# Performance work log

Measured on AMD Instinct MI355X. Metric: run time of the kernel, lower is better.

## Reference

```python
import jax, jax.numpy as jnp
import numpy as np

D_MODEL = 2048
NUM_HEADS = 16
MAX_SEQ_LEN = 2048
ROPE_BASE = 10000.0


def _rope(x, start_pos):
    # x: [B, S, D]; rotates interleaved pairs then concatenates halves,
    # exactly matching the torch module (NOT the usual interleaved output).
    B, S, D = x.shape
    theta = 1.0 / (ROPE_BASE ** (jnp.arange(0, D, 2, dtype=jnp.float32) / D))  # [D/2]
    pos = jnp.arange(start_pos, start_pos + S, dtype=jnp.float32)[:, None]      # [S,1]
    ang = pos * theta[None, :]                                                  # [S, D/2]
    cos, sin = jnp.cos(ang), jnp.sin(ang)
    x1 = x[..., 0::2]
    x2 = x[..., 1::2]
    return jnp.concatenate([x1 * cos - x2 * sin, x1 * sin + x2 * cos], axis=-1)


def setup_inputs() -> dict:
    key = jax.random.key(0)
    kx, kq, kk, kv, ko = jax.random.split(key, 5)
    B, S, D = 4, 2048, D_MODEL
    scale = 1.0 / np.sqrt(D)
    return {
        "x": jax.random.normal(kx, (B, S, D), dtype=jnp.float32),
        "w_q": jax.random.normal(kq, (D, D), dtype=jnp.float32) * scale,
        "w_k": jax.random.normal(kk, (D, D), dtype=jnp.float32) * scale,
        "w_v": jax.random.normal(kv, (D, D), dtype=jnp.float32) * scale,
        "w_o": jax.random.normal(ko, (D, D), dtype=jnp.float32) * scale,
        "start_pos": 0,
    }


def reference(x, w_q, w_k, w_v, w_o, start_pos):
    B, S, D = x.shape
    H = NUM_HEADS
    hd = D // H
    # Linear(d, d, bias=False): y = x @ W^T
    Q = _rope(x @ w_q.T, start_pos)
    K = _rope(x @ w_k.T, start_pos)
    V = x @ w_v.T
    q = Q.reshape(B, S, H, hd).transpose(0, 2, 1, 3)  # [B,H,S,hd]
    k = K.reshape(B, S, H, hd).transpose(0, 2, 1, 3)
    v = V.reshape(B, S, H, hd).transpose(0, 2, 1, 3)
    # cache=None path: kv_len == S
    attn = jnp.einsum("bhqd,bhkd->bhqk", q, k) / jnp.sqrt(jnp.float32(hd))
    # causal mask: key j attends only if j <= i + (kv_len - seq_len); here offset=0
    kv_len = k.shape[2]
    offset = kv_len - S
    i = jnp.arange(S)[:, None]
    j = jnp.arange(kv_len)[None, :]
    attn = jnp.where(j > i + offset, jnp.float32(-jnp.inf), attn)
    attn = jax.nn.softmax(attn, axis=-1)
    # dropout: inference mode (identity)
    out = jnp.einsum("bhqk,bhkd->bhqd", attn, v)
    out = out.transpose(0, 2, 1, 3).reshape(B, S, D)
    output = out @ w_o.T
    return (output, k, v)
```

## Files before the change

### kernel.cpp

```cpp
#include <hip/hip_runtime.h>
#include <hip/hip_bf16.h>

typedef __attribute__((ext_vector_type(4))) float f32x4;
typedef __attribute__((ext_vector_type(8))) short s16x8;

#define SEQ 2048
#define DM  2048
#define NH  16
#define HD  128

__device__ __forceinline__ unsigned short f2b(float f){
  unsigned int u = __builtin_bit_cast(unsigned int, f);
  u += 0x7fffu + ((u >> 16) & 1u);
  return (unsigned short)(u >> 16);
}
__device__ __forceinline__ float b2f(unsigned short h){
  unsigned int u = ((unsigned int)h) << 16;
  return __builtin_bit_cast(float, u);
}
__device__ __forceinline__ f32x4 mfma16(s16x8 a, s16x8 b, f32x4 c){
  return __builtin_amdgcn_mfma_f32_16x16x32_bf16(a, b, c, 0, 0, 0);
}

__global__ __launch_bounds__(256)
void convert_kernel(const float* __restrict__ x,  const float* __restrict__ wq,
                    const float* __restrict__ wk, const float* __restrict__ wv,
                    const float* __restrict__ wo,
                    unsigned short* __restrict__ xb,
                    unsigned short* __restrict__ wfused,
                    unsigned short* __restrict__ wob)
{
  size_t e = ((size_t)blockIdx.x * 256 + threadIdx.x) * 8;
  const float* src; unsigned short* dst;
  if (e < 16777216){ src = x + e; dst = xb + e; }
  else if (e < 29360128){
    size_t o = e - 16777216;
    int sel = (int)(o >> 22);
    const float* w = sel == 0 ? wq : (sel == 1 ? wk : wv);
    src = w + (o & 4194303); dst = wfused + o;
  } else {
    size_t o = e - 29360128;
    src = wo + o; dst = wob + o;
  }
  float4 a = ((const float4*)src)[0];
  float4 b = ((const float4*)src)[1];
  s16x8 v;
  v[0]=(short)f2b(a.x); v[1]=(short)f2b(a.y); v[2]=(short)f2b(a.z); v[3]=(short)f2b(a.w);
  v[4]=(short)f2b(b.x); v[5]=(short)f2b(b.y); v[6]=(short)f2b(b.z); v[7]=(short)f2b(b.w);
  *(s16x8*)dst = v;
}

template<int MODE>
__global__ __launch_bounds__(512, 1)
void gemm8(const unsigned short* __restrict__ A,
           const unsigned short* __restrict__ B,
           unsigned short* __restrict__ qr, unsigned short* __restrict__ kr,
           float* __restrict__ koutf,
           float* __restrict__ voutf, unsigned short* __restrict__ vt,
           float* __restrict__ outf, const int* __restrict__ sp)
{
  extern __shared__ char lds[];
  const int tid  = threadIdx.x;
  const int lane = tid & 63;
  const int w    = tid >> 6;
  const int wr   = w >> 2;
  const int wc   = w & 3;
  const int l15  = lane & 15;
  const int lhi  = lane >> 4;
  const int rq   = lhi << 2;

  int bid = blockIdx.x;
  int x8 = bid & 7, j = bid >> 3;
  int mb, nb;
  if (MODE == 0){ nb = 3*x8 + (j % 3); mb = j / 3; }
  else          { nb = x8;             mb = j; }
  const int m0 = mb * 256, n0 = nb * 256;

  const int sp0 = (MODE == 0) ? sp[0] : 0;

  const unsigned short* Abase = A + (size_t)m0 * 2048;
  const unsigned short* Bbase = B + (size_t)n0 * 2048;

  f32x4 accL[4][4] = {};
  f32x4 accH[4][4] = {};

  auto STAGE = [&](const unsigned short* gbase, int slotoff, int t){
    #pragma unroll
    for (int r2 = 0; r2 < 2; r2++){
      int p  = r2*8192 + w*1024 + (lane << 4);
      int lo = p ^ (((p >> 7) & 3) << 4);
      int row = lo >> 6, colB = lo & 63;
      __builtin_amdgcn_global_load_lds(
        (const __attribute__((address_space(1))) void*)
          (gbase + (size_t)row*2048 + t*32 + (colB >> 1)),
        (__attribute__((address_space(3))) void*)(lds + slotoff + r2*8192 + w*1024),
        16, 0, 0);
    }
  };
  auto LDA = [&](const char* base, int i0, s16x8* dst){
    #pragma unroll
    for (int i = 0; i < 4; i++){
      int row = wr*128 + (i0 + i)*16 + l15;
      int off = row*64 + lhi*16;
      dst[i] = *(const s16x8*)(base + (off ^ (((row >> 1) & 3) << 4)));
    }
  };
  auto LDB = [&](const char* base, s16x8* dst){
    #pragma unroll
    for (int j2 = 0; j2 < 4; j2++){
      int row = wc*64 + j2*16 + l15;
      int off = row*64 + lhi*16;
      dst[j2] = *(const s16x8*)(base + (off ^ (((row >> 1) & 3) << 4)));
    }
  };
  auto MM = [&](s16x8* a, s16x8* b, f32x4 (&ac)[4][4]){
    __builtin_amdgcn_s_setprio(1);
    #pragma unroll
    for (int i = 0; i < 4; i++)
      #pragma unroll
      for (int j2 = 0; j2 < 4; j2++)
        ac[i][j2] = mfma16(a[i], b[j2], ac[i][j2]);
    __builtin_amdgcn_s_setprio(0);
  };

#define TILE(T, ISSUE, VMW) { \
    const int s_ = (T) & 3; \
    const char* base_ = lds + s_*32768; \
    if (ISSUE){ \
      int so_ = (((T)+3) & 3)*32768; \
      STAGE(Abase, so_, (T)+3); \
      STAGE(Bbase, so_+16384, (T)+3); \
    } \
    s16x8 bfr[4], afL[4], afH[4]; \
    LDB(base_+16384, bfr); LDA(base_, 0, afL); LDA(base_, 4, afH); \
    MM(afL, bfr, accL); MM(afH, bfr, accH); \
    asm volatile("s_waitcnt vmcnt(" #VMW ")" ::: "memory"); \
    __builtin_amdgcn_s_barrier(); }

  STAGE(Abase, 0, 0);      STAGE(Bbase, 16384, 0);
  STAGE(Abase, 32768, 1);  STAGE(Bbase, 49152, 1);
  STAGE(Abase, 65536, 2);  STAGE(Bbase, 81920, 2);
  asm volatile("s_waitcnt vmcnt(8)" ::: "memory");
  __builtin_amdgcn_s_barrier();

  for (int t = 0; t < 61; t++) TILE(t, 1, 8);
  TILE(61, 0, 4);
  TILE(62, 0, 0);
  {
    const char* base_ = lds + 3*32768;
    s16x8 bfr[4], afL[4], afH[4];
    LDB(base_+16384, bfr); LDA(base_, 0, afL); LDA(base_, 4, afH);
    MM(afL, bfr, accL); MM(afH, bfr, accH);
  }
#undef TILE

  if (MODE == 1){
    #pragma unroll
    for (int h2 = 0; h2 < 2; h2++){
      f32x4 (&ac)[4][4] = h2 ? accH : accL;
      int ibase = h2 * 4;
      #pragma unroll
      for (int i = 0; i < 4; i++)
        #pragma unroll
        for (int r = 0; r < 4; r++){
          int m = m0 + wr*128 + (ibase+i)*16 + rq + r;
          #pragma unroll
          for (int j2 = 0; j2 < 4; j2++)
            outf[(size_t)m*DM + n0 + wc*64 + j2*16 + l15] = ac[i][j2][r];
        }
    }
    return;
  }

  const int b  = m0 >> 11;
  const int s0 = m0 & 2047;

  if (nb < 16){
    const bool isK = (nb >= 8);
    unsigned short* dqk = isK ? kr : qr;
    const int fbase = (nb & 7) * 128;
    const int odd = lane & 1;

    __syncthreads();
    float2* T2 = (float2*)lds;
    float2* T1 = (float2*)(lds + 32768);
    for (int idx = tid; idx < 5120; idx += 512){
      int fl = idx & 127;
      float th = exp2f(-(float)(fbase + fl) * (13.287712379549449f / 1024.0f));
      float sn, cn;
      if (idx < 4096){
        __sincosf((float)(idx >> 7) * th, &sn, &cn);
        T2[idx] = make_float2(cn, sn);
      } else {
        int sh = (idx - 4096) >> 7;
        __sincosf((float)(sp0 + s0 + sh*32) * th, &sn, &cn);
        T1[idx - 4096] = make_float2(cn, sn);
      }
    }
    __syncthreads();

    #pragma unroll
    for (int h2 = 0; h2 < 2; h2++){
      f32x4 (&ac)[4][4] = h2 ? accH : accL;
      int ibase = h2 * 4;
      #pragma unroll
      for (int i = 0; i < 4; i++){
        #pragma unroll
        for (int r = 0; r < 4; r++){
          int srow = wr*128 + (ibase+i)*16 + rq + r;
          int s  = s0 + srow;
          int sh = srow >> 5, sl = srow & 31;
          #pragma unroll
          for (int j2 = 0; j2 < 4; j2++){
            float v  = ac[i][j2][r];
            float vx = __shfl_xor(v, 1);
            int nn_loc = wc*64 + j2*16 + l15;
            int fl = nn_loc >> 1;
            float2 a1 = T1[sh*128 + fl];
            float2 a2 = T2[sl*128 + fl];
            float cn = a1.x*a2.x - a1.y*a2.y;
            float sn = a1.y*a2.x + a1.x*a2.y;
            float x1 = odd ? vx : v;
            float x2 = odd ? v  : vx;
            float ov = odd ? (x1*sn + x2*cn) : (x1*cn - x2*sn);
            int c = fbase + fl + (odd ? 1024 : 0);
            size_t adr = ((size_t)(b*NH + (c >> 7))*SEQ + s)*HD + (c & 127);
            dqk[adr] = f2b(ov);
            if (isK) koutf[adr] = ov;
          }
        }
      }
    }
  } else {
    #pragma unroll
    for (int h2 = 0; h2 < 2; h2++){
      f32x4 (&ac)[4][4] = h2 ? accH : accL;
      int ibase = h2 * 4;
      #pragma unroll
      for (int i = 0; i < 4; i++){
        int sb = s0 + wr*128 + (ibase+i)*16 + rq;
        #pragma unroll
        for (int j2 = 0; j2 < 4; j2++){
          int d = (nb - 16)*256 + wc*64 + j2*16 + l15;
          int h = d >> 7, dd = d & 127;
          size_t vb = ((size_t)(b*NH + h)*SEQ + sb)*HD + dd;
          #pragma unroll
          for (int r = 0; r < 4; r++)
            voutf[vb + (size_t)r*HD] = ac[i][j2][r];
          ushort4 pk;
          pk.x = f2b(ac[i][j2][0]); pk.y = f2b(ac[i][j2][1]);
          pk.z = f2b(ac[i][j2][2]); pk.w = f2b(ac[i][j2][3]);
          *(ushort4*)(vt + ((size_t)(b*NH + h)*HD + dd)*SEQ + sb) = pk;
        }
      }
    }
  }
}

__global__ __launch_bounds__(256)
void attn_kernel(const unsigned short* __restrict__ qr,
                 const unsigned short* __restrict__ kr,
                 const unsigned short* __restrict__ vt,
                 unsigned short* __restrict__ attnout)
{
  const int pair = blockIdx.x;
  const int bh   = blockIdx.y;
  const int tid  = threadIdx.x;
  const int lane = tid & 63;
  const int w    = tid >> 6;

  __shared__ __align__(16) char Klds[64 * 256];
  __shared__ __align__(16) char Vlds[128 * 144];
  __shared__ __align__(16) char Plds[4][16 * 144];

  const int l15 = lane & 15;
  const int lhi = lane >> 4;
  const int rq  = lhi << 2;
  char* pw = &Plds[w][0];

  s16x8 ones;
  #pragma unroll
  for (int i = 0; i < 8; i++) ones[i] = (short)0x3F80;

  const int b = bh >> 4, h = bh & 15;

  for (int ph = 0; ph < 2; ph++){
    const int qtile = ph ? (31 - pair) : pair;
    const int q0w = qtile*64 + w*16;

    s16x8 qf[4];
    const unsigned short* qbase = qr + ((size_t)bh*SEQ + q0w + l15) * HD + lhi*8;
    #pragma unroll
    for (int c = 0; c < 4; c++) qf[c] = *(const s16x8*)(qbase + c*32);

    f32x4 o[8] = {};
    f32x4 osum = {};
    float mrow[4] = {-1e30f,-1e30f,-1e30f,-1e30f};

    const int ntiles = qtile + 1;
    for (int t = 0; t < ntiles; t++){
      const int kv0 = t * 64;
      __syncthreads();
      {
        int r = tid >> 2, q4 = tid & 3;
        const unsigned short* src = kr + ((size_t)bh*SEQ + kv0 + r) * HD + q4*32;
        int sw = (r & 15) << 4;
        char* drow = Klds + r*256;
        #pragma unroll
        for (int k = 0; k < 4; k++)
          *(s16x8*)(drow + ((q4*64 + k*16) ^ sw)) = *(const s16x8*)(src + k*8);
      }
      {
        int r = tid >> 1, h2 = tid & 1;
        const unsigned short* src = vt + ((size_t)bh*HD + r) * SEQ + kv0 + h2*32;
        char* drow = Vlds + r*144 + h2*64;
        #pragma unroll
        for (int k = 0; k < 4; k++)
          *(s16x8*)(drow + k*16) = *(const s16x8*)(src + k*8);
      }
      __syncthreads();

      f32x4 st[4];
      #pragma unroll
      for (int j = 0; j < 4; j++) st[j] = (f32x4){0.f,0.f,0.f,0.f};
      #pragma unroll
      for (int j = 0; j < 4; j++){
        int krw = j*16 + l15;
        int sw  = (krw & 15) << 4;
        #pragma unroll
        for (int c = 0; c < 4; c++){
          s16x8 kf = *(const s16x8*)(Klds + krw*256 + ((c*64 + lhi*16) ^ sw));
          st[j] = mfma16(qf[c], kf, st[j]);
        }
      }

      const float sc = 0.08838834764831845f;
      #pragma unroll
      for (int j = 0; j < 4; j++)
        #pragma unroll
        for (int r = 0; r < 4; r++){
          int qrow = q0w + rq + r;
          int kvc  = kv0 + j*16 + l15;
          st[j][r] = (kvc > qrow) ? -1e30f : st[j][r] * sc;
        }

      float mt[4];
      #pragma unroll
      for (int r = 0; r < 4; r++)
        mt[r] = fmaxf(fmaxf(st[0][r], st[1][r]), fmaxf(st[2][r], st[3][r]));
      #pragma unroll
      for (int mk = 1; mk < 16; mk <<= 1)
        #pragma unroll
        for (int r = 0; r < 4; r++) mt[r] = fmaxf(mt[r], __shfl_xor(mt[r], mk));

      int ok = 1;
      #pragma unroll
      for (int r = 0; r < 4; r++) ok &= (mt[r] <= mrow[r] + 8.0f) ? 1 : 0;
      if (!__all(ok)){
        float al[4];
        #pragma unroll
        for (int r = 0; r < 4; r++){
          float mn = fmaxf(mrow[r], mt[r]);
          al[r] = __expf(mrow[r] - mn);
          mrow[r] = mn;
        }
        #pragma unroll
        for (int c = 0; c < 8; c++)
          #pragma unroll
          for (int r = 0; r < 4; r++) o[c][r] *= al[r];
        #pragma unroll
        for (int r = 0; r < 4; r++) osum[r] *= al[r];
      }

      #pragma unroll
      for (int r = 0; r < 4; r++){
        char* prb = pw + (rq + r)*144;
        #pragma unroll
        for (int j = 0; j < 4; j++){
          float p = __expf(st[j][r] - mrow[r]);
          *(unsigned short*)(prb + (j*16 + l15)*2) = f2b(p);
        }
      }

      asm volatile("s_waitcnt lgkmcnt(0)" ::: "memory");

      #pragma unroll
      for (int ks = 0; ks < 2; ks++){
        s16x8 pa = *(const s16x8*)(pw + l15*144 + ks*64 + lhi*16);
        #pragma unroll
        for (int c = 0; c < 8; c++){
          int d = c*16 + l15;
          s16x8 vf = *(const s16x8*)(Vlds + d*144 + ks*64 + lhi*16);
          o[c] = mfma16(pa, vf, o[c]);
        }
        osum = mfma16(pa, ones, osum);
      }
    }

    #pragma unroll
    for (int r = 0; r < 4; r++){
      float inv = 1.0f / osum[r];
      int s2 = q0w + rq + r;
      size_t base = ((size_t)(b*SEQ + s2)) * DM + h*HD;
      #pragma unroll
      for (int c = 0; c < 8; c++)
        attnout[base + c*16 + l15] = f2b(o[c][r] * inv);
    }
  }
}

extern "C" void kernel_launch(void* const* d_in, const int* in_sizes, int n_in,
                              void* d_out, int out_size, void* d_ws, size_t ws_size,
                              hipStream_t stream)
{
  const float* x  = (const float*)d_in[0];
  const float* wq = (const float*)d_in[1];
  const float* wk = (const float*)d_in[2];
  const float* wv = (const float*)d_in[3];
  const float* wo = (const float*)d_in[4];
  const int*   sp = (const int*)d_in[5];

  float* out  = (float*)d_out;
  float* kout = out + 16777216;
  float* vout = out + 33554432;

  char* ws = (char*)d_ws;
  unsigned short* xb      = (unsigned short*)ws;
  unsigned short* wfused  = (unsigned short*)(ws + 33554432);
  unsigned short* wob     = (unsigned short*)(ws + 58720256);
  unsigned short* qr      = (unsigned short*)(ws + 67108864);
  unsigned short* kr      = (unsigned short*)(ws + 100663296);
  unsigned short* vt      = (unsigned short*)(ws + 134217728);
  unsigned short* attnout = (unsigned short*)ws;

  hipFuncSetAttribute((const void*)gemm8<0>,
                      hipFuncAttributeMaxDynamicSharedMemorySize, 131072);
  hipFuncSetAttribute((const void*)gemm8<1>,
                      hipFuncAttributeMaxDynamicSharedMemorySize, 131072);

  convert_kernel<<<16384, 256, 0, stream>>>(x, wq, wk, wv, wo, xb, wfused, wob);
  gemm8<0><<<768, 512, 131072, stream>>>(xb, wfused, qr, kr, kout,
                                         vout, vt, nullptr, sp);
  attn_kernel<<<dim3(16, 64), 256, 0, stream>>>(qr, kr, vt, attnout);
  gemm8<1><<<256, 512, 131072, stream>>>(attnout, wob, nullptr, nullptr,
                                         nullptr, nullptr, nullptr, out, nullptr);
}
```

Measured before the change: 521.3 us.

## Restructure GEMM main loop to double-buffered K=64 tiles with interleaved loads

Replaces the four-slot K=32 LDS ring with a two-slot ring of K=64 tiles (64KB each). Global-to-LDS loads for the next tile are split into quarters and interleaved between MFMA phases, and each phase is separated by barriers. A new XOR swizzle matches the 128-byte row pitch. The aim is fewer loop iterations and finer overlap of loads with compute, at the cost of more barriers per tile and a shallower prefetch depth.

```diff
diff --git a/kernel.cpp b/kernel.cpp
--- a/kernel.cpp
+++ b/kernel.cpp
@@ -70,10 +70,10 @@
   const int rq   = lhi << 2;
 
   int bid = blockIdx.x;
-  int x8 = bid & 7, j = bid >> 3;
+  int x8 = bid & 7, jb = bid >> 3;
   int mb, nb;
-  if (MODE == 0){ nb = 3*x8 + (j % 3); mb = j / 3; }
-  else          { nb = x8;             mb = j; }
+  if (MODE == 0){ nb = 3*x8 + (jb % 3); mb = jb / 3; }
+  else          { nb = x8;              mb = jb; }
   const int m0 = mb * 256, n0 = nb * 256;
 
   const int sp0 = (MODE == 0) ? sp[0] : 0;
@@ -81,94 +81,96 @@
   const unsigned short* Abase = A + (size_t)m0 * 2048;
   const unsigned short* Bbase = B + (size_t)n0 * 2048;
 
-  f32x4 accL[4][4] = {};
-  f32x4 accH[4][4] = {};
-
-  auto STAGE = [&](const unsigned short* gbase, int slotoff, int t){
-    #pragma unroll
-    for (int r2 = 0; r2 < 2; r2++){
-      int p  = r2*8192 + w*1024 + (lane << 4);
-      int lo = p ^ (((p >> 7) & 3) << 4);
-      int row = lo >> 6, colB = lo & 63;
-      __builtin_amdgcn_global_load_lds(
-        (const __attribute__((address_space(1))) void*)
-          (gbase + (size_t)row*2048 + t*32 + (colB >> 1)),
-        (__attribute__((address_space(3))) void*)(lds + slotoff + r2*8192 + w*1024),
-        16, 0, 0);
-    }
+  f32x4 acc[8][4] = {};
+  s16x8 af[4], af2[4], bf[4];
+
+  const int rowl0 = w*8 + (lane >> 3);
+  const int colel = (((lane & 7) ^ ((lane >> 3) & 7)) << 3);
+  const int kbsw  = (l15 & 7) << 4;
+  const int ldst0 = w*1024 + (lane << 4);
+
+  auto GLOAD = [&](const unsigned short* g, int opoff, int h, int r2, int t, int sl){
+    __builtin_amdgcn_global_load_lds(
+      (const __attribute__((address_space(1))) void*)
+        (g + (size_t)(h*128 + r2*64 + rowl0)*2048 + t*64 + colel),
+      (__attribute__((address_space(3))) void*)
+        (lds + sl*65536 + opoff + h*16384 + r2*8192 + ldst0),
+      16, 0, 0);
   };
-  auto LDA = [&](const char* base, int i0, s16x8* dst){
-    #pragma unroll
-    for (int i = 0; i < 4; i++){
-      int row = wr*128 + (i0 + i)*16 + l15;
-      int off = row*64 + lhi*16;
-      dst[i] = *(const s16x8*)(base + (off ^ (((row >> 1) & 3) << 4)));
-    }
+  auto LDA4 = [&](int sl, int ks, int f0, s16x8* d){
+    const char* base = lds + sl*65536;
+    int kb = (ks*64 + lhi*16) ^ kbsw;
+    #pragma unroll
+    for (int i = 0; i < 4; i++)
+      d[i] = *(const s16x8*)(base + (wr*128 + (f0+i)*16 + l15)*128 + kb);
   };
-  auto LDB = [&](const char* base, s16x8* dst){
-    #pragma unroll
-    for (int j2 = 0; j2 < 4; j2++){
-      int row = wc*64 + j2*16 + l15;
-      int off = row*64 + lhi*16;
-      dst[j2] = *(const s16x8*)(base + (off ^ (((row >> 1) & 3) << 4)));
-    }
+  auto LDB4 = [&](int sl, int ks, s16x8* d){
+    const char* base = lds + sl*65536 + 32768;
+    int kb = (ks*64 + lhi*16) ^ kbsw;
+    #pragma unroll
+    for (int j2 = 0; j2 < 4; j2++)
+      d[j2] = *(const s16x8*)(base + (wc*64 + j2*16 + l15)*128 + kb);
   };
-  auto MM = [&](s16x8* a, s16x8* b, f32x4 (&ac)[4][4]){
+  auto MM16 = [&](s16x8* a, s16x8* b, int i0){
     __builtin_amdgcn_s_setprio(1);
     #pragma unroll
     for (int i = 0; i < 4; i++)
       #pragma unroll
       for (int j2 = 0; j2 < 4; j2++)
-        ac[i][j2] = mfma16(a[i], b[j2], ac[i][j2]);
+        acc[i0+i][j2] = mfma16(a[i], b[j2], acc[i0+i][j2]);
     __builtin_amdgcn_s_setprio(0);
   };
 
-#define TILE(T, ISSUE, VMW) { \
-    const int s_ = (T) & 3; \
-    const char* base_ = lds + s_*32768; \
-    if (ISSUE){ \
-      int so_ = (((T)+3) & 3)*32768; \
-      STAGE(Abase, so_, (T)+3); \
-      STAGE(Bbase, so_+16384, (T)+3); \
-    } \
-    s16x8 bfr[4], afL[4], afH[4]; \
-    LDB(base_+16384, bfr); LDA(base_, 0, afL); LDA(base_, 4, afH); \
-    MM(afL, bfr, accL); MM(afH, bfr, accH); \
-    asm volatile("s_waitcnt vmcnt(" #VMW ")" ::: "memory"); \
-    __builtin_amdgcn_s_barrier(); }
-
-  STAGE(Abase, 0, 0);      STAGE(Bbase, 16384, 0);
-  STAGE(Abase, 32768, 1);  STAGE(Bbase, 49152, 1);
-  STAGE(Abase, 65536, 2);  STAGE(Bbase, 81920, 2);
-  asm volatile("s_waitcnt vmcnt(8)" ::: "memory");
-  __builtin_amdgcn_s_barrier();
-
-  for (int t = 0; t < 61; t++) TILE(t, 1, 8);
-  TILE(61, 0, 4);
-  TILE(62, 0, 0);
+#define BAR __builtin_amdgcn_s_barrier()
+#define VM2 asm volatile("s_waitcnt vmcnt(2)" ::: "memory")
+#define VM0 asm volatile("s_waitcnt vmcnt(0)" ::: "memory")
+
+  GLOAD(Bbase,32768,0,0,0,0); GLOAD(Bbase,32768,0,1,0,0);
+  GLOAD(Bbase,32768,1,0,0,0); GLOAD(Bbase,32768,1,1,0,0);
+  GLOAD(Abase,0,0,0,0,0);     GLOAD(Abase,0,1,0,0,0);
+  GLOAD(Abase,0,0,1,0,0);     GLOAD(Abase,0,1,1,0,0);
+  VM2; BAR;
+
+  #pragma unroll 2
+  for (int t = 0; t < 31; t++){
+    const int sl = t & 1, ns = sl ^ 1;
+    LDB4(sl,0,bf); LDA4(sl,0,0,af);
+    GLOAD(Bbase,32768,0,0,t+1,ns); GLOAD(Bbase,32768,0,1,t+1,ns);
+    BAR; MM16(af,bf,0); VM2; BAR;
+    LDA4(sl,0,4,af2);
+    GLOAD(Bbase,32768,1,0,t+1,ns); GLOAD(Bbase,32768,1,1,t+1,ns);
+    BAR; MM16(af2,bf,4); BAR;
+    LDB4(sl,1,bf); LDA4(sl,1,0,af);
+    GLOAD(Abase,0,0,0,t+1,ns); GLOAD(Abase,0,1,0,t+1,ns);
+    BAR; MM16(af,bf,0); BAR;
+    LDA4(sl,1,4,af2);
+    GLOAD(Abase,0,0,1,t+1,ns); GLOAD(Abase,0,1,1,t+1,ns);
+    BAR; MM16(af2,bf,4); VM2; BAR;
+  }
   {
-    const char* base_ = lds + 3*32768;
-    s16x8 bfr[4], afL[4], afH[4];
-    LDB(base_+16384, bfr); LDA(base_, 0, afL); LDA(base_, 4, afH);
-    MM(afL, bfr, accL); MM(afH, bfr, accH);
-  }
-#undef TILE
+    LDB4(1,0,bf); LDA4(1,0,0,af);
+    BAR; MM16(af,bf,0); VM0; BAR;
+    LDA4(1,0,4,af2);
+    BAR; MM16(af2,bf,4); BAR;
+    LDB4(1,1,bf); LDA4(1,1,0,af);
+    BAR; MM16(af,bf,0); BAR;
+    LDA4(1,1,4,af2);
+    MM16(af2,bf,4);
+  }
+#undef BAR
+#undef VM2
+#undef VM0
 
   if (MODE == 1){
     #pragma unroll
-    for (int h2 = 0; h2 < 2; h2++){
-      f32x4 (&ac)[4][4] = h2 ? accH : accL;
-      int ibase = h2 * 4;
-      #pragma unroll
-      for (int i = 0; i < 4; i++)
-        #pragma unroll
-        for (int r = 0; r < 4; r++){
-          int m = m0 + wr*128 + (ibase+i)*16 + rq + r;
-          #pragma unroll
-          for (int j2 = 0; j2 < 4; j2++)
-            outf[(size_t)m*DM + n0 + wc*64 + j2*16 + l15] = ac[i][j2][r];
-        }
-    }
+    for (int i = 0; i < 8; i++)
+      #pragma unroll
+      for (int r = 0; r < 4; r++){
+        int m = m0 + wr*128 + i*16 + rq + r;
+        #pragma unroll
+        for (int j2 = 0; j2 < 4; j2++)
+          outf[(size_t)m*DM + n0 + wc*64 + j2*16 + l15] = acc[i][j2][r];
+      }
     return;
   }
 
@@ -200,58 +202,48 @@
     __syncthreads();
 
     #pragma unroll
-    for (int h2 = 0; h2 < 2; h2++){
-      f32x4 (&ac)[4][4] = h2 ? accH : accL;
-      int ibase = h2 * 4;
-      #pragma unroll
-      for (int i = 0; i < 4; i++){
-        #pragma unroll
-        for (int r = 0; r < 4; r++){
-          int srow = wr*128 + (ibase+i)*16 + rq + r;
-          int s  = s0 + srow;
-          int sh = srow >> 5, sl = srow & 31;
-          #pragma unroll
-          for (int j2 = 0; j2 < 4; j2++){
-            float v  = ac[i][j2][r];
-            float vx = __shfl_xor(v, 1);
-            int nn_loc = wc*64 + j2*16 + l15;
-            int fl = nn_loc >> 1;
-            float2 a1 = T1[sh*128 + fl];
-            float2 a2 = T2[sl*128 + fl];
-            float cn = a1.x*a2.x - a1.y*a2.y;
-            float sn = a1.y*a2.x + a1.x*a2.y;
-            float x1 = odd ? vx : v;
-            float x2 = odd ? v  : vx;
-            float ov = odd ? (x1*sn + x2*cn) : (x1*cn - x2*sn);
-            int c = fbase + fl + (odd ? 1024 : 0);
-            size_t adr = ((size_t)(b*NH + (c >> 7))*SEQ + s)*HD + (c & 127);
-            dqk[adr] = f2b(ov);
-            if (isK) koutf[adr] = ov;
-          }
+    for (int i = 0; i < 8; i++){
+      #pragma unroll
+      for (int r = 0; r < 4; r++){
+        int srow = wr*128 + i*16 + rq + r;
+        int s  = s0 + srow;
+        int sh = srow >> 5, sl2 = srow & 31;
+        #pragma unroll
+        for (int j2 = 0; j2 < 4; j2++){
+          float v  = acc[i][j2][r];
+          float vx = __shfl_xor(v, 1);
+          int nn_loc = wc*64 + j2*16 + l15;
+          int fl = nn_loc >> 1;
+          float2 a1 = T1[sh*128 + fl];
+          float2 a2 = T2[sl2*128 + fl];
+          float cn = a1.x*a2.x - a1.y*a2.y;
+          float sn = a1.y*a2.x + a1.x*a2.y;
+          float x1 = odd ? vx : v;
+          float x2 = odd ? v  : vx;
+          float ov = odd ? (x1*sn + x2*cn) : (x1*cn - x2*sn);
+          int c = fbase + fl + (odd ? 1024 : 0);
+          size_t adr = ((size_t)(b*NH + (c >> 7))*SEQ + s)*HD + (c & 127);
+          dqk[adr] = f2b(ov);
+          if (isK) koutf[adr] = ov;
         }
       }
     }
   } else {
     #pragma unroll
-    for (int h2 = 0; h2 < 2; h2++){
-      f32x4 (&ac)[4][4] = h2 ? accH : accL;
-      int ibase = h2 * 4;
-      #pragma unroll
-      for (int i = 0; i < 4; i++){
-        int sb = s0 + wr*128 + (ibase+i)*16 + rq;
-        #pragma unroll
-        for (int j2 = 0; j2 < 4; j2++){
-          int d = (nb - 16)*256 + wc*64 + j2*16 + l15;
-          int h = d >> 7, dd = d & 127;
-          size_t vb = ((size_t)(b*NH + h)*SEQ + sb)*HD + dd;
-          #pragma unroll
-          for (int r = 0; r < 4; r++)
-            voutf[vb + (size_t)r*HD] = ac[i][j2][r];
-          ushort4 pk;
-          pk.x = f2b(ac[i][j2][0]); pk.y = f2b(ac[i][j2][1]);
-          pk.z = f2b(ac[i][j2][2]); pk.w = f2b(ac[i][j2][3]);
-          *(ushort4*)(vt + ((size_t)(b*NH + h)*HD + dd)*SEQ + sb) = pk;
-        }
+    for (int i = 0; i < 8; i++){
+      int sb = s0 + wr*128 + i*16 + rq;
+      #pragma unroll
+      for (int j2 = 0; j2 < 4; j2++){
+        int d = (nb - 16)*256 + wc*64 + j2*16 + l15;
+        int h = d >> 7, dd = d & 127;
+        size_t vb = ((size_t)(b*NH + h)*SEQ + sb)*HD + dd;
+        #pragma unroll
+        for (int r = 0; r < 4; r++)
+          voutf[vb + (size_t)r*HD] = acc[i][j2][r];
+        ushort4 pk;
+        pk.x = f2b(acc[i][j2][0]); pk.y = f2b(acc[i][j2][1]);
+        pk.z = f2b(acc[i][j2][2]); pk.w = f2b(acc[i][j2][3]);
+        *(ushort4*)(vt + ((size_t)(b*NH + h)*HD + dd)*SEQ + sb) = pk;
       }
     }
   }
```

Result: slower. 593.7 us (+13.9%).

## Restage QKV GEMM epilogue through LDS for coalesced vector stores

Applied to the files above, without the earlier changes.

The QKV projection epilogue used to write RoPE'd Q/K and V (fp32 and bf16 transposed) straight from MFMA accumulator fragments, producing scattered 2- and 4-byte stores. It now dumps 64-row chunks of the accumulators into a padded LDS tile. Threads then reread whole row segments, apply RoPE on contiguous pairs, and issue 16-byte vector stores. The V transpose is likewise built from LDS columns so it writes contiguous runs. This adds extra LDS traffic and two barriers per chunk, and it uses more shared memory.

```diff
diff --git a/kernel.cpp b/kernel.cpp
--- a/kernel.cpp
+++ b/kernel.cpp
@@ -70,10 +70,10 @@
   const int rq   = lhi << 2;
 
   int bid = blockIdx.x;
-  int x8 = bid & 7, j = bid >> 3;
+  int x8 = bid & 7, jb = bid >> 3;
   int mb, nb;
-  if (MODE == 0){ nb = 3*x8 + (j % 3); mb = j / 3; }
-  else          { nb = x8;             mb = j; }
+  if (MODE == 0){ nb = 3*x8 + (jb % 3); mb = jb / 3; }
+  else          { nb = x8;              mb = jb; }
   const int m0 = mb * 256, n0 = nb * 256;
 
   const int sp0 = (MODE == 0) ? sp[0] : 0;
@@ -174,19 +174,20 @@
 
   const int b  = m0 >> 11;
   const int s0 = m0 & 2047;
+  const int P  = 260;
+  float*  LF = (float*)lds;
+  float2* T2 = (float2*)(lds + 81920);
+  float2* T1 = (float2*)(lds + 114688);
+
+  __syncthreads();
 
   if (nb < 16){
     const bool isK = (nb >= 8);
     unsigned short* dqk = isK ? kr : qr;
-    const int fbase = (nb & 7) * 128;
-    const int odd = lane & 1;
-
-    __syncthreads();
-    float2* T2 = (float2*)lds;
-    float2* T1 = (float2*)(lds + 32768);
+    const int hq = nb & 7;
     for (int idx = tid; idx < 5120; idx += 512){
       int fl = idx & 127;
-      float th = exp2f(-(float)(fbase + fl) * (13.287712379549449f / 1024.0f));
+      float th = exp2f(-(float)(hq*128 + fl) * (13.287712379549449f / 1024.0f));
       float sn, cn;
       if (idx < 4096){
         __sincosf((float)(idx >> 7) * th, &sn, &cn);
@@ -199,60 +200,111 @@
     }
     __syncthreads();
 
-    #pragma unroll
-    for (int h2 = 0; h2 < 2; h2++){
-      f32x4 (&ac)[4][4] = h2 ? accH : accL;
-      int ibase = h2 * 4;
-      #pragma unroll
-      for (int i = 0; i < 4; i++){
-        #pragma unroll
-        for (int r = 0; r < 4; r++){
-          int srow = wr*128 + (ibase+i)*16 + rq + r;
-          int s  = s0 + srow;
-          int sh = srow >> 5, sl = srow & 31;
+    const int row_l = tid >> 3;
+    const int tr    = tid & 7;
+    #pragma unroll 1
+    for (int ck = 0; ck < 4; ck++){
+      if (wr == (ck >> 1)){
+        f32x4 (&ac)[4][4] = (ck & 1) ? accH : accL;
+        #pragma unroll
+        for (int i = 0; i < 4; i++)
           #pragma unroll
-          for (int j2 = 0; j2 < 4; j2++){
-            float v  = ac[i][j2][r];
-            float vx = __shfl_xor(v, 1);
-            int nn_loc = wc*64 + j2*16 + l15;
-            int fl = nn_loc >> 1;
-            float2 a1 = T1[sh*128 + fl];
-            float2 a2 = T2[sl*128 + fl];
-            float cn = a1.x*a2.x - a1.y*a2.y;
-            float sn = a1.y*a2.x + a1.x*a2.y;
-            float x1 = odd ? vx : v;
-            float x2 = odd ? v  : vx;
-            float ov = odd ? (x1*sn + x2*cn) : (x1*cn - x2*sn);
-            int c = fbase + fl + (odd ? 1024 : 0);
-            size_t adr = ((size_t)(b*NH + (c >> 7))*SEQ + s)*HD + (c & 127);
-            dqk[adr] = f2b(ov);
-            if (isK) koutf[adr] = ov;
-          }
-        }
-      }
+          for (int j2 = 0; j2 < 4; j2++)
+            #pragma unroll
+            for (int r = 0; r < 4; r++)
+              LF[(i*16 + rq + r)*P + wc*64 + j2*16 + l15] = ac[i][j2][r];
+      }
+      __syncthreads();
+
+      int s_local = ck*64 + row_l;
+      int s  = s0 + s_local;
+      int sh = s_local >> 5, sl = s_local & 31;
+      const float* rowp = LF + row_l*P + tr*32;
+      s16x8 qa0, qa1, qb0, qb1;
+      f32x4 k0[4], k1[4];
+      #pragma unroll
+      for (int q = 0; q < 8; q++){
+        f32x4 vv = *(const f32x4*)(rowp + q*4);
+        #pragma unroll
+        for (int e = 0; e < 2; e++){
+          int f16 = 2*q + e;
+          int fl  = tr*16 + f16;
+          float x1 = vv[2*e], x2 = vv[2*e+1];
+          float2 a1 = T1[sh*128 + fl];
+          float2 a2 = T2[sl*128 + fl];
+          float cn = a1.x*a2.x - a1.y*a2.y;
+          float sn = a1.y*a2.x + a1.x*a2.y;
+          float o0 = x1*cn - x2*sn;
+          float o1 = x1*sn + x2*cn;
+          if (f16 < 8){ qa0[f16] = (short)f2b(o0); qb0[f16] = (short)f2b(o1); }
+          else        { qa1[f16-8] = (short)f2b(o0); qb1[f16-8] = (short)f2b(o1); }
+          k0[f16>>2][f16&3] = o0;
+          k1[f16>>2][f16&3] = o1;
+        }
+      }
+      size_t a0 = ((size_t)(b*NH + hq    )*SEQ + s)*HD + tr*16;
+      size_t a1 = ((size_t)(b*NH + hq + 8)*SEQ + s)*HD + tr*16;
+      *(s16x8*)(dqk + a0)     = qa0;
+      *(s16x8*)(dqk + a0 + 8) = qa1;
+      *(s16x8*)(dqk + a1)     = qb0;
+      *(s16x8*)(dqk + a1 + 8) = qb1;
+      if (isK){
+        #pragma unroll
+        for (int q4 = 0; q4 < 4; q4++){
+          *(f32x4*)(koutf + a0 + q4*4) = k0[q4];
+          *(f32x4*)(koutf + a1 + q4*4) = k1[q4];
+        }
+      }
+      __syncthreads();
     }
   } else {
-    #pragma unroll
-    for (int h2 = 0; h2 < 2; h2++){
-      f32x4 (&ac)[4][4] = h2 ? accH : accL;
-      int ibase = h2 * 4;
-      #pragma unroll
-      for (int i = 0; i < 4; i++){
-        int sb = s0 + wr*128 + (ibase+i)*16 + rq;
-        #pragma unroll
-        for (int j2 = 0; j2 < 4; j2++){
-          int d = (nb - 16)*256 + wc*64 + j2*16 + l15;
-          int h = d >> 7, dd = d & 127;
-          size_t vb = ((size_t)(b*NH + h)*SEQ + sb)*HD + dd;
+    const int row_l = tid >> 3;
+    const int tr    = tid & 7;
+    const int dd2   = tid & 255;
+    const int sh2   = tid >> 8;
+    #pragma unroll 1
+    for (int ck = 0; ck < 4; ck++){
+      if (wr == (ck >> 1)){
+        f32x4 (&ac)[4][4] = (ck & 1) ? accH : accL;
+        #pragma unroll
+        for (int i = 0; i < 4; i++)
           #pragma unroll
-          for (int r = 0; r < 4; r++)
-            voutf[vb + (size_t)r*HD] = ac[i][j2][r];
-          ushort4 pk;
-          pk.x = f2b(ac[i][j2][0]); pk.y = f2b(ac[i][j2][1]);
-          pk.z = f2b(ac[i][j2][2]); pk.w = f2b(ac[i][j2][3]);
-          *(ushort4*)(vt + ((size_t)(b*NH + h)*HD + dd)*SEQ + sb) = pk;
-        }
-      }
+          for (int j2 = 0; j2 < 4; j2++)
+            #pragma unroll
+            for (int r = 0; r < 4; r++)
+              LF[(i*16 + rq + r)*P + wc*64 + j2*16 + l15] = ac[i][j2][r];
+      }
+      __syncthreads();
+
+      {
+        int s = s0 + ck*64 + row_l;
+        int dg = (nb - 16)*256 + tr*32;
+        int h = dg >> 7, dd = dg & 127;
+        const float* rowp = LF + row_l*P + tr*32;
+        float* vb = voutf + ((size_t)(b*NH + h)*SEQ + s)*HD + dd;
+        #pragma unroll
+        for (int q4 = 0; q4 < 8; q4++)
+          *(f32x4*)(vb + q4*4) = *(const f32x4*)(rowp + q4*4);
+      }
+      {
+        int dg = (nb - 16)*256 + dd2;
+        int h = dg >> 7, dd = dg & 127;
+        int sb = s0 + ck*64 + sh2*32;
+        s16x8 t0, t1, t2, t3;
+        #pragma unroll
+        for (int q = 0; q < 8; q++){
+          t0[q] = (short)f2b(LF[(sh2*32 +      q)*P + dd2]);
+          t1[q] = (short)f2b(LF[(sh2*32 +  8 + q)*P + dd2]);
+          t2[q] = (short)f2b(LF[(sh2*32 + 16 + q)*P + dd2]);
+          t3[q] = (short)f2b(LF[(sh2*32 + 24 + q)*P + dd2]);
+        }
+        unsigned short* vp = vt + ((size_t)(b*NH + h)*HD + dd)*SEQ + sb;
+        *(s16x8*)(vp)      = t0;
+        *(s16x8*)(vp + 8)  = t1;
+        *(s16x8*)(vp + 16) = t2;
+        *(s16x8*)(vp + 24) = t3;
+      }
+      __syncthreads();
     }
   }
 }
```

Result: slower. 575.8 us (+10.4%).
